# Kernel optimization log

Measured on AMD Instinct MI355X. Metric: run time of the kernel, lower is better.

The kernel has to match this reference:

```python
import jax, jax.numpy as jnp
import numpy as np

N, C, I, E = 4096, 128, 9, 10
IRREPS_OUT = [(1, 0), (3, 1)]          # (M = 2L+1, L) for target irreps 128x0e + 128x1o
PATHS = {0: (1, 2, 5), 1: (1, 3, 7)}   # (P1, P2, P3) CG path counts per output L


def setup_inputs() -> dict:
    key = jax.random.key(0)
    ks = jax.random.split(key, 32)
    inp = {}
    inp['node_feats'] = jax.random.normal(ks[0], (N, C, I), jnp.float32)
    out_dim = C * sum(m for m, _ in IRREPS_OUT)
    inp['sc'] = jax.random.normal(ks[1], (N, out_dim), jnp.float32)
    elem = jax.random.randint(ks[2], (N,), 0, E)
    inp['node_attrs'] = jax.nn.one_hot(elem, E, dtype=jnp.float32)
    i = 3
    for (M, L) in IRREPS_OUT:
        P1, P2, P3 = PATHS[L]
        # U tensors: fixed (non-learned) generalized CG basis; random stand-ins with correct shapes
        inp[f'U3_{L}'] = jax.random.normal(ks[i], (M, I, I, I, P3), jnp.float32) * 0.1; i += 1
        inp[f'U2_{L}'] = jax.random.normal(ks[i], (M, I, I, P2), jnp.float32) * 0.1; i += 1
        inp[f'U1_{L}'] = jax.random.normal(ks[i], (M, I, P1), jnp.float32) * 0.1; i += 1
        # element-indexed learned weights [E, P, C]
        inp[f'W3_{L}'] = jax.random.normal(ks[i], (E, P3, C), jnp.float32) / np.sqrt(P3); i += 1
        inp[f'W2_{L}'] = jax.random.normal(ks[i], (E, P2, C), jnp.float32) / np.sqrt(P2); i += 1
        inp[f'W1_{L}'] = jax.random.normal(ks[i], (E, P1, C), jnp.float32) / np.sqrt(P1); i += 1
        # equivariant Linear internal weight (per-irrep channel mixing)
        inp[f'Wlin_{L}'] = jax.random.normal(ks[i], (C, C), jnp.float32); i += 1
    return inp


def _symmetric_contract(x, y, U3, U2, U1, W3, W2, W1):
    """Correlation-3 symmetric CG contraction for one output irrep.
    x: [N,C,I] node feats, y: [N,E] one-hot element attrs. Returns [N,C,M]."""
    # per-node element-selected weights (gather via one-hot matmul): [N,P,C]
    w3 = jnp.einsum('ne,epc->npc', y, W3)
    w2 = jnp.einsum('ne,epc->npc', y, W2)
    w1 = jnp.einsum('ne,epc->npc', y, W1)
    # highest correlation: out[n,c,m,a,b] = sum_{i,p} U3[m,a,b,i,p] w3[n,p,c] x[n,c,i]
    xw = jnp.einsum('nci,npc->nipc', x, w3)            # [N,I,P3,C]
    out = jnp.einsum('mabip,nipc->ncmab', U3, xw)      # [N,C,M,I,I]  (largest intermediate)
    # correlation 2 term, then contract one irrep index with x
    out = out + jnp.einsum('mabp,npc->ncmab', U2, w2)
    out = jnp.einsum('ncmab,ncb->ncma', out, x)        # [N,C,M,I]
    # correlation 1 term, contract last irrep index
    out = out + jnp.einsum('map,npc->ncma', U1, w1)
    out = jnp.einsum('ncma,nca->ncm', out, x)          # [N,C,M]
    return out


def reference(node_feats, sc, node_attrs,
              U3_0, U2_0, U1_0, W3_0, W2_0, W1_0, Wlin_0,
              U3_1, U2_1, U1_1, W3_1, W2_1, W1_1, Wlin_1):
    params = {0: (U3_0, U2_0, U1_0, W3_0, W2_0, W1_0, Wlin_0),
              1: (U3_1, U2_1, U1_1, W3_1, W2_1, W1_1, Wlin_1)}
    inv_sqrt_c = 1.0 / np.sqrt(C)
    blocks = []
    for (M, L) in IRREPS_OUT:
        U3, U2, U1, W3, W2, W1, Wl = params[L]
        b = _symmetric_contract(node_feats, node_attrs, U3, U2, U1, W3, W2, W1)  # [N,C,M]
        b = jnp.einsum('ncm,cd->ndm', b, Wl) * inv_sqrt_c  # e3nn-style Linear, internal weights
        blocks.append(b.reshape(b.shape[0], -1))           # [N, C*M]
    out = jnp.concatenate(blocks, axis=-1)                 # [N, 512]
    return out + sc                                        # use_sc residual
```

## Files before the change

### kernel.cpp

```cpp
#include <hip/hip_runtime.h>

#define N_NODES 4096
#define C_CH    128
#define E_ELEM  10
#define NP      4736
#define TT      219
#define PSTRIDE (TT * 4)
#define MAXCHUNK 32
#define CHUNK_J  256

#define WS_CHE     256
#define WS_CHJ     512
#define WS_CHEND   768
#define WS_JLIST   1024
#define WS_ELEM    20480
#define WS_S31     53248
#define WS_S30     67136
#define WS_S21     70464
#define WS_S20     72128
#define WS_P       72704
#define WS_BOUT    4557824
#define WS_XS      14257152
#define WS_XS_END  36080640ull

__device__ __forceinline__ void t3_decode(int t, int& a, int& b, int& i) {
    int cnt = 0;
    for (int aa = 0; aa < 9; ++aa)
        for (int bb = aa; bb < 9; ++bb) {
            int len = 9 - bb;
            if (t < cnt + len) { a = aa; b = bb; i = bb + (t - cnt); return; }
            cnt += len;
        }
    a = b = i = 8;
}

__device__ __forceinline__ void t2_decode(int t, int& a, int& b) {
    int cnt = 0;
    for (int aa = 0; aa < 9; ++aa) {
        int len = 9 - aa;
        if (t < cnt + len) { a = aa; b = aa + (t - cnt); return; }
        cnt += len;
    }
    a = b = 8;
}

__global__ __launch_bounds__(256) void k_front(
    const float* __restrict__ attrs, int* __restrict__ elem,
    const float* __restrict__ U3_1, const float* __restrict__ U3_0,
    const float* __restrict__ U2_1, const float* __restrict__ U2_0,
    float* __restrict__ S31, float* __restrict__ S30,
    float* __restrict__ S21, float* __restrict__ S20) {
    int bid = blockIdx.x;
    if (bid >= 19) {
        int n = (bid - 19) * 256 + threadIdx.x;
        if (n >= N_NODES) return;
        const float* a = attrs + n * E_ELEM;
        float best = a[0];
        int e = 0;
#pragma unroll
        for (int k = 1; k < E_ELEM; ++k) {
            float v = a[k];
            if (v > best) { best = v; e = k; }
        }
        elem[n] = e;
        return;
    }
    int q = bid * 256 + threadIdx.x;
    if (q < 3465) {
        int m = q / 1155, r = q % 1155, t = r / 7, p = r % 7;
        int a, b, i;
        t3_decode(t, a, b, i);
#define U31(X, Y, Z) U3_1[((((m * 9 + (X)) * 9 + (Y)) * 9 + (Z)) * 7) + p]
        float s = U31(a, b, i);
        if (a == b && b == i) {}
        else if (a == b) s += U31(a, i, a) + U31(i, a, a);
        else if (b == i) s += U31(b, a, b) + U31(b, b, a);
        else s += U31(a, i, b) + U31(b, a, i) + U31(b, i, a) + U31(i, a, b) + U31(i, b, a);
#undef U31
        S31[q] = s;
        return;
    }
    q -= 3465;
    if (q < 825) {
        int t = q / 5, p = q % 5;
        int a, b, i;
        t3_decode(t, a, b, i);
#define U30(X, Y, Z) U3_0[((((X) * 9 + (Y)) * 9 + (Z)) * 5) + p]
        float s = U30(a, b, i);
        if (a == b && b == i) {}
        else if (a == b) s += U30(a, i, a) + U30(i, a, a);
        else if (b == i) s += U30(b, a, b) + U30(b, b, a);
        else s += U30(a, i, b) + U30(b, a, i) + U30(b, i, a) + U30(i, a, b) + U30(i, b, a);
#undef U30
        S30[q] = s;
        return;
    }
    q -= 825;
    if (q < 405) {
        int m = q / 135, r = q % 135, t = r / 3, p = r % 3;
        int a, b;
        t2_decode(t, a, b);
        float s = U2_1[(((m * 9 + a) * 9 + b) * 3) + p];
        if (a != b) s += U2_1[(((m * 9 + b) * 9 + a) * 3) + p];
        S21[q] = s;
        return;
    }
    q -= 405;
    if (q < 90) {
        int t = q / 2, p = q % 2;
        int a, b;
        t2_decode(t, a, b);
        float s = U2_0[((a * 9 + b) * 2) + p];
        if (a != b) s += U2_0[((b * 9 + a) * 2) + p];
        S20[q] = s;
    }
}

__global__ __launch_bounds__(1024) void k_sort(
    const int* __restrict__ elem, int* __restrict__ jlist,
    int* __restrict__ chE, int* __restrict__ chJ, int* __restrict__ chEnd) {
    __shared__ int h[E_ELEM];
    __shared__ int cur[E_ELEM];
    int tid = threadIdx.x;
    if (tid < E_ELEM) h[tid] = 0;
    __syncthreads();
    for (int n = tid; n < N_NODES; n += 1024) atomicAdd(&h[elem[n]], 1);
    for (int p = tid; p < NP; p += 1024) jlist[p] = -1;
    __syncthreads();
    if (tid == 0) {
        int ps[E_ELEM + 1];
        int s = 0;
        for (int e = 0; e < E_ELEM; ++e) {
            ps[e] = s;
            cur[e] = s;
            s += ((h[e] + 63) >> 6) << 6;
        }
        ps[E_ELEM] = s;
        int ci = 0;
        for (int e = 0; e < E_ELEM; ++e) {
            for (int ofs = ps[e]; ofs < ps[e + 1]; ofs += CHUNK_J) {
                chE[ci] = e;
                chJ[ci] = ofs;
                chEnd[ci] = ps[e + 1];
                ++ci;
            }
        }
        for (; ci < MAXCHUNK; ++ci) chE[ci] = -1;
    }
    __syncthreads();
    for (int n = tid; n < N_NODES; n += 1024) {
        int e = elem[n];
        int pos = atomicAdd(&cur[e], 1);
        jlist[pos] = n;
    }
}

__global__ __launch_bounds__(256) void k_mid(
    const float* __restrict__ S31, const float* __restrict__ S30,
    const float* __restrict__ S21, const float* __restrict__ S20,
    const float* __restrict__ U1_1, const float* __restrict__ U1_0,
    const float* __restrict__ W3_1, const float* __restrict__ W3_0,
    const float* __restrict__ W2_1, const float* __restrict__ W2_0,
    const float* __restrict__ W1_1, const float* __restrict__ W1_0,
    float* __restrict__ P,
    const float* __restrict__ x, const int* __restrict__ jlist,
    float* __restrict__ xs) {
    int bid = blockIdx.x;
    if (bid >= 1280) {
        int t = (bid - 1280) * 256 + threadIdx.x;
        int i = t % 9;
        int r = t / 9;
        int j = r % NP;
        int c = r / NP;
        int n = jlist[j];
        xs[t] = (n >= 0) ? x[((size_t)n * C_CH + c) * 9 + i] : 0.f;
        return;
    }
    int e = bid >> 7;
    int c = bid & 127;
    float* Pout = P + (size_t)bid * PSTRIDE;
    for (int q = threadIdx.x; q < PSTRIDE; q += 256) {
        int t = q >> 2, m = q & 3;
        float v;
        if (t < 9) {
            int a = t;
            v = (m == 0) ? U1_0[a] * W1_0[e * C_CH + c]
                         : U1_1[(m - 1) * 9 + a] * W1_1[e * C_CH + c];
        } else if (t < 54) {
            int t2 = t - 9;
            float s = 0.f;
            if (m == 0) {
#pragma unroll
                for (int p = 0; p < 2; ++p)
                    s = fmaf(S20[t2 * 2 + p], W2_0[(e * 2 + p) * C_CH + c], s);
            } else {
#pragma unroll
                for (int p = 0; p < 3; ++p)
                    s = fmaf(S21[((m - 1) * 45 + t2) * 3 + p], W2_1[(e * 3 + p) * C_CH + c], s);
            }
            v = s;
        } else {
            int t3 = t - 54;
            float s = 0.f;
            if (m == 0) {
#pragma unroll
                for (int p = 0; p < 5; ++p)
                    s = fmaf(S30[t3 * 5 + p], W3_0[(e * 5 + p) * C_CH + c], s);
            } else {
#pragma unroll
                for (int p = 0; p < 7; ++p)
                    s = fmaf(S31[((m - 1) * 165 + t3) * 7 + p], W3_1[(e * 7 + p) * C_CH + c], s);
            }
            v = s;
        }
        Pout[q] = v;
    }
}

__device__ __forceinline__ void poly_eval1(const float* __restrict__ sP,
                                           const float (&xv)[9], float (&acc)[4]) {
    const float* p1 = sP;
    const float* p2 = sP + 9 * 4;
    const float* p3 = sP + 54 * 4;
    int i2 = 0, i3 = 0;
#pragma unroll
    for (int a = 0; a < 9; ++a) {
        float4 q1 = *(const float4*)(p1 + a * 4);
        float xa = xv[a];
        acc[0] = fmaf(q1.x, xa, acc[0]);
        acc[1] = fmaf(q1.y, xa, acc[1]);
        acc[2] = fmaf(q1.z, xa, acc[2]);
        acc[3] = fmaf(q1.w, xa, acc[3]);
        __builtin_amdgcn_sched_barrier(0);
#pragma unroll
        for (int b = a; b < 9; ++b) {
            float4 q2 = *(const float4*)(p2 + i2 * 4);
            ++i2;
            float m2 = xv[a] * xv[b];
            acc[0] = fmaf(q2.x, m2, acc[0]);
            acc[1] = fmaf(q2.y, m2, acc[1]);
            acc[2] = fmaf(q2.z, m2, acc[2]);
            acc[3] = fmaf(q2.w, m2, acc[3]);
#pragma unroll
            for (int i = b; i < 9; ++i) {
                float4 q3 = *(const float4*)(p3 + i3 * 4);
                ++i3;
                float m3 = m2 * xv[i];
                acc[0] = fmaf(q3.x, m3, acc[0]);
                acc[1] = fmaf(q3.y, m3, acc[1]);
                acc[2] = fmaf(q3.z, m3, acc[2]);
                acc[3] = fmaf(q3.w, m3, acc[3]);
            }
            __builtin_amdgcn_sched_barrier(0);
        }
    }
}

__global__ __launch_bounds__(256) void k_poly(
    const float* __restrict__ xs, const int* __restrict__ chE,
    const int* __restrict__ chJ, const int* __restrict__ chEnd,
    const float* __restrict__ P, float* __restrict__ bout) {
    int ci = blockIdx.y;
    int e = chE[ci];
    if (e < 0) return;
    e = __builtin_amdgcn_readfirstlane(e);
    int c = blockIdx.x;
    const float* __restrict__ Pg = P + (size_t)(e * C_CH + c) * PSTRIDE;

    const int end = chEnd[ci];
    const int j = chJ[ci] + threadIdx.x;
    if (j >= end) return;

    float xv[9];
    const float* px = xs + ((size_t)c * NP + j) * 9;
#pragma unroll
    for (int i = 0; i < 9; ++i) xv[i] = px[i];
    float acc[4] = {};
    poly_eval1(Pg, xv, acc);
#pragma unroll
    for (int m = 0; m < 4; ++m) bout[(size_t)(c * 4 + m) * NP + j] = acc[m];
}

__global__ __launch_bounds__(256) void k_linear(
    const float* __restrict__ bout, const int* __restrict__ jlist,
    const float* __restrict__ Wl0, const float* __restrict__ Wl1,
    const float* __restrict__ sc, float* __restrict__ out) {
    const int s  = blockIdx.y >> 2;
    const int dg = blockIdx.y & 3;
    const int jj = threadIdx.x & 63;
    const int wv = threadIdx.x >> 6;
    const int dbase = __builtin_amdgcn_readfirstlane(dg * 32 + wv * 8);
    const int j = blockIdx.x * 64 + jj;
    const float* __restrict__ Wl = (s == 0) ? Wl0 : Wl1;
    const float* __restrict__ brow = bout + (size_t)s * NP + j;

    float acc[8];
#pragma unroll
    for (int k = 0; k < 8; ++k) acc[k] = 0.f;

#pragma unroll 1
    for (int cc0 = 0; cc0 < C_CH; cc0 += 32) {
        float bv[32];
#pragma unroll
        for (int t = 0; t < 32; ++t)
            bv[t] = brow[(size_t)(cc0 + t) * 4 * NP];
#pragma unroll
        for (int t = 0; t < 32; ++t) {
            const float* wrow = Wl + (cc0 + t) * C_CH + dbase;
#pragma unroll
            for (int k = 0; k < 8; ++k) acc[k] = fmaf(bv[t], wrow[k], acc[k]);
        }
    }

    const int n = jlist[j];
    if (n < 0) return;
    const float inv = 0.08838834764831845f;
#pragma unroll
    for (int k = 0; k < 8; ++k) {
        int d = dbase + k;
        int col = (s == 0) ? d : (128 + d * 3 + (s - 1));
        out[n * 512 + col] = fmaf(acc[k], inv, sc[n * 512 + col]);
    }
}

extern "C" void kernel_launch(void* const* d_in, const int* in_sizes, int n_in,
                              void* d_out, int out_size, void* d_ws, size_t ws_size,
                              hipStream_t stream) {
    const float* x     = (const float*)d_in[0];
    const float* sc    = (const float*)d_in[1];
    const float* attrs = (const float*)d_in[2];
    const float* U3_0 = (const float*)d_in[3];
    const float* U2_0 = (const float*)d_in[4];
    const float* U1_0 = (const float*)d_in[5];
    const float* W3_0 = (const float*)d_in[6];
    const float* W2_0 = (const float*)d_in[7];
    const float* W1_0 = (const float*)d_in[8];
    const float* Wl0  = (const float*)d_in[9];
    const float* U3_1 = (const float*)d_in[10];
    const float* U2_1 = (const float*)d_in[11];
    const float* U1_1 = (const float*)d_in[12];
    const float* W3_1 = (const float*)d_in[13];
    const float* W2_1 = (const float*)d_in[14];
    const float* W1_1 = (const float*)d_in[15];
    const float* Wl1  = (const float*)d_in[16];

    char* ws = (char*)d_ws;
    int* chE     = (int*)(ws + WS_CHE);
    int* chJ     = (int*)(ws + WS_CHJ);
    int* chEnd   = (int*)(ws + WS_CHEND);
    int* jlist   = (int*)(ws + WS_JLIST);
    int* elem    = (int*)(ws + WS_ELEM);
    float* S31   = (float*)(ws + WS_S31);
    float* S30   = (float*)(ws + WS_S30);
    float* S21   = (float*)(ws + WS_S21);
    float* S20   = (float*)(ws + WS_S20);
    float* P     = (float*)(ws + WS_P);
    float* bout  = (float*)(ws + WS_BOUT);
    float* xs    = (float*)(ws + WS_XS);

    k_front<<<35, 256, 0, stream>>>(attrs, elem, U3_1, U3_0, U2_1, U2_0,
                                    S31, S30, S21, S20);
    k_sort<<<1, 1024, 0, stream>>>(elem, jlist, chE, chJ, chEnd);
    k_mid<<<1280 + (C_CH * NP * 9) / 256, 256, 0, stream>>>(
        S31, S30, S21, S20, U1_1, U1_0, W3_1, W3_0, W2_1, W2_0, W1_1, W1_0,
        P, x, jlist, xs);
    k_poly<<<dim3(128, MAXCHUNK), 256, 0, stream>>>(xs, chE, chJ, chEnd, P, bout);
    k_linear<<<dim3(NP / 64, 16), 256, 0, stream>>>(bout, jlist, Wl0, Wl1, sc,
                                                    (float*)d_out);
}
```

Baseline: 91.66 us.

## Merge front and sort kernels; evaluate two nodes per thread in poly kernel

Folds element argmax, histogram and bucketing into one setup block using wave ballots, and runs the S-tensor symmetrisation in the remaining blocks of the same launch. This removes one kernel launch and the global elem round-trip. The poly kernel now handles two nodes per thread with chunks of 512, so each P coefficient load is reused across two nodes. The cost is fewer blocks and threads in flight, plus higher register pressure.

```diff
diff --git a/kernel.cpp b/kernel.cpp
--- a/kernel.cpp
+++ b/kernel.cpp
@@ -7,13 +7,12 @@
 #define TT      219
 #define PSTRIDE (TT * 4)
 #define MAXCHUNK 32
-#define CHUNK_J  256
+#define CHUNK_J  512
 
 #define WS_CHE     256
 #define WS_CHJ     512
 #define WS_CHEND   768
 #define WS_JLIST   1024
-#define WS_ELEM    20480
 #define WS_S31     53248
 #define WS_S30     67136
 #define WS_S21     70464
@@ -44,28 +43,86 @@
     a = b = 8;
 }
 
-__global__ __launch_bounds__(256) void k_front(
-    const float* __restrict__ attrs, int* __restrict__ elem,
+__global__ __launch_bounds__(1024) void k_setup(
+    const float* __restrict__ attrs, int* __restrict__ jlist,
+    int* __restrict__ chE, int* __restrict__ chJ, int* __restrict__ chEnd,
     const float* __restrict__ U3_1, const float* __restrict__ U3_0,
     const float* __restrict__ U2_1, const float* __restrict__ U2_0,
     float* __restrict__ S31, float* __restrict__ S30,
     float* __restrict__ S21, float* __restrict__ S20) {
-    int bid = blockIdx.x;
-    if (bid >= 19) {
-        int n = (bid - 19) * 256 + threadIdx.x;
-        if (n >= N_NODES) return;
-        const float* a = attrs + n * E_ELEM;
-        float best = a[0];
-        int e = 0;
-#pragma unroll
-        for (int k = 1; k < E_ELEM; ++k) {
-            float v = a[k];
-            if (v > best) { best = v; e = k; }
-        }
-        elem[n] = e;
+    const int bid = blockIdx.x;
+    const int tid = threadIdx.x;
+    if (bid == 0) {
+        __shared__ int selem[N_NODES];
+        __shared__ int h[E_ELEM];
+        __shared__ int cur[E_ELEM];
+        if (tid < E_ELEM) h[tid] = 0;
+        __syncthreads();
+        const int lane = tid & 63;
+        for (int it = 0; it < N_NODES / 1024; ++it) {
+            int n = it * 1024 + tid;
+            const float* a = attrs + n * E_ELEM;
+            float best = a[0];
+            int e = 0;
+#pragma unroll
+            for (int k = 1; k < E_ELEM; ++k) {
+                float v = a[k];
+                if (v > best) { best = v; e = k; }
+            }
+            selem[n] = e;
+#pragma unroll
+            for (int e0 = 0; e0 < E_ELEM; ++e0) {
+                unsigned long long m = __ballot(e == e0);
+                if (m) {
+                    int lead = __ffsll(m) - 1;
+                    if (lane == lead) atomicAdd(&h[e0], __popcll(m));
+                }
+            }
+        }
+        for (int p = tid; p < NP; p += 1024) jlist[p] = -1;
+        __syncthreads();
+        if (tid == 0) {
+            int ps[E_ELEM + 1];
+            int s = 0;
+            for (int e = 0; e < E_ELEM; ++e) {
+                ps[e] = s;
+                cur[e] = s;
+                s += ((h[e] + 63) >> 6) << 6;
+            }
+            ps[E_ELEM] = s;
+            int ci = 0;
+            for (int e = 0; e < E_ELEM; ++e) {
+                for (int ofs = ps[e]; ofs < ps[e + 1]; ofs += CHUNK_J) {
+                    chE[ci] = e;
+                    chJ[ci] = ofs;
+                    chEnd[ci] = ps[e + 1];
+                    ++ci;
+                }
+            }
+            for (; ci < MAXCHUNK; ++ci) chE[ci] = -1;
+        }
+        __syncthreads();
+        for (int it = 0; it < N_NODES / 1024; ++it) {
+            int n = it * 1024 + tid;
+            int e = selem[n];
+#pragma unroll
+            for (int e0 = 0; e0 < E_ELEM; ++e0) {
+                unsigned long long m = __ballot(e == e0);
+                if (m) {
+                    int lead = __ffsll(m) - 1;
+                    int base = 0;
+                    if (lane == lead) base = atomicAdd(&cur[e0], __popcll(m));
+                    base = __shfl(base, lead, 64);
+                    if (e == e0) {
+                        int r = __popcll(m & ((1ull << lane) - 1ull));
+                        jlist[base + r] = n;
+                    }
+                }
+            }
+        }
         return;
     }
-    int q = bid * 256 + threadIdx.x;
+    int q = (bid - 1) * 1024 + tid;
     if (q < 3465) {
         int m = q / 1155, r = q % 1155, t = r / 7, p = r % 7;
         int a, b, i;
@@ -113,45 +170,6 @@
         float s = U2_0[((a * 9 + b) * 2) + p];
         if (a != b) s += U2_0[((b * 9 + a) * 2) + p];
         S20[q] = s;
-    }
-}
-
-__global__ __launch_bounds__(1024) void k_sort(
-    const int* __restrict__ elem, int* __restrict__ jlist,
-    int* __restrict__ chE, int* __restrict__ chJ, int* __restrict__ chEnd) {
-    __shared__ int h[E_ELEM];
-    __shared__ int cur[E_ELEM];
-    int tid = threadIdx.x;
-    if (tid < E_ELEM) h[tid] = 0;
-    __syncthreads();
-    for (int n = tid; n < N_NODES; n += 1024) atomicAdd(&h[elem[n]], 1);
-    for (int p = tid; p < NP; p += 1024) jlist[p] = -1;
-    __syncthreads();
-    if (tid == 0) {
-        int ps[E_ELEM + 1];
-        int s = 0;
-        for (int e = 0; e < E_ELEM; ++e) {
-            ps[e] = s;
-            cur[e] = s;
-            s += ((h[e] + 63) >> 6) << 6;
-        }
-        ps[E_ELEM] = s;
-        int ci = 0;
-        for (int e = 0; e < E_ELEM; ++e) {
-            for (int ofs = ps[e]; ofs < ps[e + 1]; ofs += CHUNK_J) {
-                chE[ci] = e;
-                chJ[ci] = ofs;
-                chEnd[ci] = ps[e + 1];
-                ++ci;
-            }
-        }
-        for (; ci < MAXCHUNK; ++ci) chE[ci] = -1;
-    }
-    __syncthreads();
-    for (int n = tid; n < N_NODES; n += 1024) {
-        int e = elem[n];
-        int pos = atomicAdd(&cur[e], 1);
-        jlist[pos] = n;
     }
 }
 
@@ -217,8 +235,8 @@
     }
 }
 
-__device__ __forceinline__ void poly_eval1(const float* __restrict__ sP,
-                                           const float (&xv)[9], float (&acc)[4]) {
+__device__ __forceinline__ void poly_eval2(const float* __restrict__ sP,
+                                           const float (&xv)[2][9], float (&acc)[2][4]) {
     const float* p1 = sP;
     const float* p2 = sP + 9 * 4;
     const float* p3 = sP + 54 * 4;
@@ -226,30 +244,40 @@
 #pragma unroll
     for (int a = 0; a < 9; ++a) {
         float4 q1 = *(const float4*)(p1 + a * 4);
-        float xa = xv[a];
-        acc[0] = fmaf(q1.x, xa, acc[0]);
-        acc[1] = fmaf(q1.y, xa, acc[1]);
-        acc[2] = fmaf(q1.z, xa, acc[2]);
-        acc[3] = fmaf(q1.w, xa, acc[3]);
+#pragma unroll
+        for (int u = 0; u < 2; ++u) {
+            float xa = xv[u][a];
+            acc[u][0] = fmaf(q1.x, xa, acc[u][0]);
+            acc[u][1] = fmaf(q1.y, xa, acc[u][1]);
+            acc[u][2] = fmaf(q1.z, xa, acc[u][2]);
+            acc[u][3] = fmaf(q1.w, xa, acc[u][3]);
+        }
         __builtin_amdgcn_sched_barrier(0);
 #pragma unroll
         for (int b = a; b < 9; ++b) {
             float4 q2 = *(const float4*)(p2 + i2 * 4);
             ++i2;
-            float m2 = xv[a] * xv[b];
-            acc[0] = fmaf(q2.x, m2, acc[0]);
-            acc[1] = fmaf(q2.y, m2, acc[1]);
-            acc[2] = fmaf(q2.z, m2, acc[2]);
-            acc[3] = fmaf(q2.w, m2, acc[3]);
+            float m2[2];
+#pragma unroll
+            for (int u = 0; u < 2; ++u) {
+                m2[u] = xv[u][a] * xv[u][b];
+                acc[u][0] = fmaf(q2.x, m2[u], acc[u][0]);
+                acc[u][1] = fmaf(q2.y, m2[u], acc[u][1]);
+                acc[u][2] = fmaf(q2.z, m2[u], acc[u][2]);
+                acc[u][3] = fmaf(q2.w, m2[u], acc[u][3]);
+            }
 #pragma unroll
             for (int i = b; i < 9; ++i) {
                 float4 q3 = *(const float4*)(p3 + i3 * 4);
                 ++i3;
-                float m3 = m2 * xv[i];
-                acc[0] = fmaf(q3.x, m3, acc[0]);
-                acc[1] = fmaf(q3.y, m3, acc[1]);
-                acc[2] = fmaf(q3.z, m3, acc[2]);
-                acc[3] = fmaf(q3.w, m3, acc[3]);
+#pragma unroll
+                for (int u = 0; u < 2; ++u) {
+                    float m3 = m2[u] * xv[u][i];
+                    acc[u][0] = fmaf(q3.x, m3, acc[u][0]);
+                    acc[u][1] = fmaf(q3.y, m3, acc[u][1]);
+                    acc[u][2] = fmaf(q3.z, m3, acc[u][2]);
+                    acc[u][3] = fmaf(q3.w, m3, acc[u][3]);
+                }
             }
             __builtin_amdgcn_sched_barrier(0);
         }
@@ -268,17 +296,24 @@
     const float* __restrict__ Pg = P + (size_t)(e * C_CH + c) * PSTRIDE;
 
     const int end = chEnd[ci];
-    const int j = chJ[ci] + threadIdx.x;
-    if (j >= end) return;
-
-    float xv[9];
-    const float* px = xs + ((size_t)c * NP + j) * 9;
-#pragma unroll
-    for (int i = 0; i < 9; ++i) xv[i] = px[i];
-    float acc[4] = {};
-    poly_eval1(Pg, xv, acc);
-#pragma unroll
-    for (int m = 0; m < 4; ++m) bout[(size_t)(c * 4 + m) * NP + j] = acc[m];
+    const int jA = chJ[ci] + threadIdx.x;
+    const int jB = jA + 256;
+    const bool vA = jA < end, vB = jB < end;
+    if (!vA) return;
+
+    float xv[2][9];
+    const float* pA = xs + ((size_t)c * NP + jA) * 9;
+    const float* pB = xs + ((size_t)c * NP + (vB ? jB : jA)) * 9;
+#pragma unroll
+    for (int i = 0; i < 9; ++i) { xv[0][i] = pA[i]; xv[1][i] = pB[i]; }
+    float acc[2][4] = {};
+    poly_eval2(Pg, xv, acc);
+#pragma unroll
+    for (int m = 0; m < 4; ++m) bout[(size_t)(c * 4 + m) * NP + jA] = acc[0][m];
+    if (vB) {
+#pragma unroll
+        for (int m = 0; m < 4; ++m) bout[(size_t)(c * 4 + m) * NP + jB] = acc[1][m];
+    }
 }
 
 __global__ __launch_bounds__(256) void k_linear(
@@ -349,7 +384,6 @@
     int* chJ     = (int*)(ws + WS_CHJ);
     int* chEnd   = (int*)(ws + WS_CHEND);
     int* jlist   = (int*)(ws + WS_JLIST);
-    int* elem    = (int*)(ws + WS_ELEM);
     float* S31   = (float*)(ws + WS_S31);
     float* S30   = (float*)(ws + WS_S30);
     float* S21   = (float*)(ws + WS_S21);
@@ -358,9 +392,8 @@
     float* bout  = (float*)(ws + WS_BOUT);
     float* xs    = (float*)(ws + WS_XS);
 
-    k_front<<<35, 256, 0, stream>>>(attrs, elem, U3_1, U3_0, U2_1, U2_0,
-                                    S31, S30, S21, S20);
-    k_sort<<<1, 1024, 0, stream>>>(elem, jlist, chE, chJ, chEnd);
+    k_setup<<<6, 1024, 0, stream>>>(attrs, jlist, chE, chJ, chEnd,
+                                    U3_1, U3_0, U2_1, U2_0, S31, S30, S21, S20);
     k_mid<<<1280 + (C_CH * NP * 9) / 256, 256, 0, stream>>>(
         S31, S30, S21, S20, U1_1, U1_0, W3_1, W3_0, W2_1, W2_0, W1_1, W1_0,
         P, x, jlist, xs);
```

New measurement: 105.3 us. 1.15x slower.

## Fuse sort into fold kernel and drop transposed x staging buffer

Applied to the files above, without the earlier changes.

Merges the single-block element sort and the per-(element,channel) polynomial fold into one launch, with block 0 doing the sort and the other blocks building P. It also removes the gathered/transposed copy of x (about 22 MB written then re-read); k_poly now indexes x directly through jlist. This saves one kernel launch and a large memory round-trip. The cost is strided, uncoalesced reads of x in k_poly, since consecutive threads now touch different nodes, plus 1024-thread blocks for the fold work.

```diff
diff --git a/kernel.cpp b/kernel.cpp
--- a/kernel.cpp
+++ b/kernel.cpp
@@ -20,8 +20,6 @@
 #define WS_S20     72128
 #define WS_P       72704
 #define WS_BOUT    4557824
-#define WS_XS      14257152
-#define WS_XS_END  36080640ull
 
 __device__ __forceinline__ void t3_decode(int t, int& a, int& b, int& i) {
     int cnt = 0;
@@ -116,70 +114,59 @@
     }
 }
 
-__global__ __launch_bounds__(1024) void k_sort(
+__global__ __launch_bounds__(1024) void k_sortfold(
     const int* __restrict__ elem, int* __restrict__ jlist,
-    int* __restrict__ chE, int* __restrict__ chJ, int* __restrict__ chEnd) {
-    __shared__ int h[E_ELEM];
-    __shared__ int cur[E_ELEM];
-    int tid = threadIdx.x;
-    if (tid < E_ELEM) h[tid] = 0;
-    __syncthreads();
-    for (int n = tid; n < N_NODES; n += 1024) atomicAdd(&h[elem[n]], 1);
-    for (int p = tid; p < NP; p += 1024) jlist[p] = -1;
-    __syncthreads();
-    if (tid == 0) {
-        int ps[E_ELEM + 1];
-        int s = 0;
-        for (int e = 0; e < E_ELEM; ++e) {
-            ps[e] = s;
-            cur[e] = s;
-            s += ((h[e] + 63) >> 6) << 6;
-        }
-        ps[E_ELEM] = s;
-        int ci = 0;
-        for (int e = 0; e < E_ELEM; ++e) {
-            for (int ofs = ps[e]; ofs < ps[e + 1]; ofs += CHUNK_J) {
-                chE[ci] = e;
-                chJ[ci] = ofs;
-                chEnd[ci] = ps[e + 1];
-                ++ci;
-            }
-        }
-        for (; ci < MAXCHUNK; ++ci) chE[ci] = -1;
-    }
-    __syncthreads();
-    for (int n = tid; n < N_NODES; n += 1024) {
-        int e = elem[n];
-        int pos = atomicAdd(&cur[e], 1);
-        jlist[pos] = n;
-    }
-}
-
-__global__ __launch_bounds__(256) void k_mid(
+    int* __restrict__ chE, int* __restrict__ chJ, int* __restrict__ chEnd,
     const float* __restrict__ S31, const float* __restrict__ S30,
     const float* __restrict__ S21, const float* __restrict__ S20,
     const float* __restrict__ U1_1, const float* __restrict__ U1_0,
     const float* __restrict__ W3_1, const float* __restrict__ W3_0,
     const float* __restrict__ W2_1, const float* __restrict__ W2_0,
     const float* __restrict__ W1_1, const float* __restrict__ W1_0,
-    float* __restrict__ P,
-    const float* __restrict__ x, const int* __restrict__ jlist,
-    float* __restrict__ xs) {
-    int bid = blockIdx.x;
-    if (bid >= 1280) {
-        int t = (bid - 1280) * 256 + threadIdx.x;
-        int i = t % 9;
-        int r = t / 9;
-        int j = r % NP;
-        int c = r / NP;
-        int n = jlist[j];
-        xs[t] = (n >= 0) ? x[((size_t)n * C_CH + c) * 9 + i] : 0.f;
-        return;
-    }
-    int e = bid >> 7;
-    int c = bid & 127;
-    float* Pout = P + (size_t)bid * PSTRIDE;
-    for (int q = threadIdx.x; q < PSTRIDE; q += 256) {
+    float* __restrict__ P) {
+    const int bid = blockIdx.x;
+    const int tid = threadIdx.x;
+    if (bid == 0) {
+        __shared__ int h[E_ELEM];
+        __shared__ int cur[E_ELEM];
+        if (tid < E_ELEM) h[tid] = 0;
+        __syncthreads();
+        for (int n = tid; n < N_NODES; n += 1024) atomicAdd(&h[elem[n]], 1);
+        for (int p = tid; p < NP; p += 1024) jlist[p] = -1;
+        __syncthreads();
+        if (tid == 0) {
+            int ps[E_ELEM + 1];
+            int s = 0;
+            for (int e = 0; e < E_ELEM; ++e) {
+                ps[e] = s;
+                cur[e] = s;
+                s += ((h[e] + 63) >> 6) << 6;
+            }
+            ps[E_ELEM] = s;
+            int ci = 0;
+            for (int e = 0; e < E_ELEM; ++e) {
+                for (int ofs = ps[e]; ofs < ps[e + 1]; ofs += CHUNK_J) {
+                    chE[ci] = e;
+                    chJ[ci] = ofs;
+                    chEnd[ci] = ps[e + 1];
+                    ++ci;
+                }
+            }
+            for (; ci < MAXCHUNK; ++ci) chE[ci] = -1;
+        }
+        __syncthreads();
+        for (int n = tid; n < N_NODES; n += 1024) {
+            int e = elem[n];
+            int pos = atomicAdd(&cur[e], 1);
+            jlist[pos] = n;
+        }
+        return;
+    }
+    int fb = bid - 1;
+    int e = fb >> 7;
+    int c = fb & 127;
+    float* Pout = P + (size_t)fb * PSTRIDE;
+    for (int q = tid; q < PSTRIDE; q += 1024) {
         int t = q >> 2, m = q & 3;
         float v;
         if (t < 9) {
@@ -257,9 +244,10 @@
 }
 
 __global__ __launch_bounds__(256) void k_poly(
-    const float* __restrict__ xs, const int* __restrict__ chE,
-    const int* __restrict__ chJ, const int* __restrict__ chEnd,
-    const float* __restrict__ P, float* __restrict__ bout) {
+    const float* __restrict__ x, const int* __restrict__ jlist,
+    const int* __restrict__ chE, const int* __restrict__ chJ,
+    const int* __restrict__ chEnd, const float* __restrict__ P,
+    float* __restrict__ bout) {
     int ci = blockIdx.y;
     int e = chE[ci];
     if (e < 0) return;
@@ -270,9 +258,11 @@
     const int end = chEnd[ci];
     const int j = chJ[ci] + threadIdx.x;
     if (j >= end) return;
+    const int n = jlist[j];
+    if (n < 0) return;
 
     float xv[9];
-    const float* px = xs + ((size_t)c * NP + j) * 9;
+    const float* px = x + ((size_t)n * C_CH + c) * 9;
 #pragma unroll
     for (int i = 0; i < 9; ++i) xv[i] = px[i];
     float acc[4] = {};
@@ -356,15 +346,14 @@
     float* S20   = (float*)(ws + WS_S20);
     float* P     = (float*)(ws + WS_P);
     float* bout  = (float*)(ws + WS_BOUT);
-    float* xs    = (float*)(ws + WS_XS);
 
     k_front<<<35, 256, 0, stream>>>(attrs, elem, U3_1, U3_0, U2_1, U2_0,
                                     S31, S30, S21, S20);
-    k_sort<<<1, 1024, 0, stream>>>(elem, jlist, chE, chJ, chEnd);
-    k_mid<<<1280 + (C_CH * NP * 9) / 256, 256, 0, stream>>>(
-        S31, S30, S21, S20, U1_1, U1_0, W3_1, W3_0, W2_1, W2_0, W1_1, W1_0,
-        P, x, jlist, xs);
-    k_poly<<<dim3(128, MAXCHUNK), 256, 0, stream>>>(xs, chE, chJ, chEnd, P, bout);
+    k_sortfold<<<1281, 1024, 0, stream>>>(elem, jlist, chE, chJ, chEnd,
+                                          S31, S30, S21, S20, U1_1, U1_0,
+                                          W3_1, W3_0, W2_1, W2_0, W1_1, W1_0, P);
+    k_poly<<<dim3(128, MAXCHUNK), 256, 0, stream>>>(x, jlist, chE, chJ, chEnd,
+                                                    P, bout);
     k_linear<<<dim3(NP / 64, 16), 256, 0, stream>>>(bout, jlist, Wl0, Wl1, sc,
                                                     (float*)d_out);
 }
```

New measurement: 77.00 us. 1.19x faster.
